# Performance work log

Hardware: AMD Instinct MI355X
Metric: run time of the kernel (lower is better)

## Reference

```python
import jax, jax.numpy as jnp
import numpy as np

B, T, C, H = 4, 2048, 1024, 16
HD = C // H

def setup_inputs() -> dict:
    key = jax.random.key(0)
    ks = jax.random.split(key, 9)
    s = 1.0 / np.sqrt(C)
    return {
        'x':  jax.random.normal(ks[0], (B, T, C), jnp.float32),
        'Wq': jax.random.normal(ks[1], (C, C), jnp.float32) * s,
        'bq': jnp.zeros((C,), jnp.float32),
        'Wk': jax.random.normal(ks[2], (C, C), jnp.float32) * s,
        'bk': jnp.zeros((C,), jnp.float32),
        'Wv': jax.random.normal(ks[3], (C, C), jnp.float32) * s,
        'bv': jnp.zeros((C,), jnp.float32),
        'Wo': jax.random.normal(ks[4], (C, C), jnp.float32) * s,
        'bo': jnp.zeros((C,), jnp.float32),
    }

def reference(x, Wq, bq, Wk, bk, Wv, bv, Wo, bo):
    Bx, Tx, Cx = x.shape
    # projections (torch Linear: x @ W.T + b); split heads -> (B,H,T,HD)
    def heads(y):
        return y.reshape(Bx, Tx, H, HD).transpose(0, 2, 1, 3)
    q = heads(x @ Wq.T + bq)
    k = heads(x @ Wk.T + bk)
    v = heads(x @ Wv.T + bv)
    # NOTE: original scales by 1/sqrt(embedding_dim), not head_dim
    scale = 1.0 / jnp.sqrt(jnp.asarray(Cx, x.dtype))
    att = jnp.einsum('bhqd,bhkd->bhqk', q, k) * scale
    mask = jnp.tril(jnp.ones((Tx, Tx), dtype=bool))
    att = jnp.where(mask, att, jnp.asarray(-jnp.inf, att.dtype))
    att = jax.nn.softmax(att, axis=-1)
    y = jnp.einsum('bhqk,bhkd->bhqd', att, v)
    y = y.transpose(0, 2, 1, 3).reshape(Bx, Tx, Cx)
    return y @ Wo.T + bo
```

## Files before the change

### kernel.cpp

```cpp
#include <hip/hip_runtime.h>
#include <hip/hip_bf16.h>
#include <stdint.h>

#define NB 4
#define NT 2048
#define NC 1024
#define NH 16
#define NHD 64
#define NM (NB*NT)

typedef __attribute__((ext_vector_type(8))) __bf16 bf16x8;
typedef __attribute__((ext_vector_type(4))) float floatx4;
typedef __attribute__((ext_vector_type(8))) unsigned short ushortx8;

#define AS1(p) ((const __attribute__((address_space(1))) void*)(p))
#define AS3(p) ((__attribute__((address_space(3))) void*)(p))

__device__ __forceinline__ unsigned short f2bf(float f) {
    union { float f; unsigned int u; } v; v.f = f;
    unsigned int u = v.u;
    return (unsigned short)((u + 0x7FFFu + ((u >> 16) & 1u)) >> 16);
}
__device__ __forceinline__ unsigned int pk2(float lo, float hi) {
    union { float f; unsigned int u; } a, b; a.f = hi; b.f = lo;
    return __builtin_amdgcn_perm(a.u, b.u, 0x07060302u);
}


__global__ void cast_all(const float* __restrict__ x,
                         const float* __restrict__ w0, const float* __restrict__ w1,
                         const float* __restrict__ w2, const float* __restrict__ w3,
                         unsigned short* __restrict__ xo,
                         unsigned short* __restrict__ o0, unsigned short* __restrict__ o1,
                         unsigned short* __restrict__ o2, unsigned short* __restrict__ o3)
{
    const int wid  = (blockIdx.x * blockDim.x + threadIdx.x) >> 6;
    const int lane = threadIdx.x & 63;
    const float* in; unsigned short* out; int tile;
    if (wid < 16384) { in = x; out = xo; tile = wid; }
    else {
        const int t = wid - 16384;
        tile = t & 2047;
        switch (t >> 11) {
            case 0: in = w0; out = o0; break;
            case 1: in = w1; out = o1; break;
            case 2: in = w2; out = o2; break;
            default: in = w3; out = o3; break;
        }
    }
    const int R = tile >> 5, C = tile & 31;
    const float* src = in + ((size_t)(R*16 + (lane >> 2)))*1024 + C*32 + (lane & 3)*8;
    const floatx4 v0 = *(const floatx4*)src;
    const floatx4 v1 = *(const floatx4*)(src + 4);
    ushortx8 o;
    o[0] = f2bf(v0[0]); o[1] = f2bf(v0[1]); o[2] = f2bf(v0[2]); o[3] = f2bf(v0[3]);
    o[4] = f2bf(v1[0]); o[5] = f2bf(v1[1]); o[6] = f2bf(v1[2]); o[7] = f2bf(v1[3]);
    *(ushortx8*)&out[(size_t)tile*512 + (((lane & 3)*16 + (lane >> 2)))*8] = o;
}

#define TM 128
#define BK 32

template<int MODE, int TN_>
__device__ __forceinline__ void gemm_core(
    const unsigned short* __restrict__ A,
    const unsigned short* __restrict__ W,
    const float* __restrict__ bias,
    void* __restrict__ Out,
    unsigned short* As, unsigned short* Bs,
    int m_base, int n_base, float oscale)
{
    constexpr int NI  = TN_ / 32;
    constexpr int TB4 = TN_ / 64;
    constexpr int BHALF = TN_ * 32;

    const int tid  = threadIdx.x;
    const int lane = tid & 63;
    const int wv   = tid >> 6;
    const int quad = lane >> 4;
    const int l16  = lane & 15;
    const int wm = (wv >> 1) * 64;
    const int wn = (wv & 1) * (TN_ / 2);

    floatx4 acc[4][NI];
    #pragma unroll
    for (int i = 0; i < 4; ++i)
        #pragma unroll
        for (int j = 0; j < NI; ++j)
            acc[i][j] = (floatx4){0.f, 0.f, 0.f, 0.f};

    const int kct = NC >> 5;

    const unsigned short* At = A + ((size_t)((m_base >> 4) + wv*2) * kct) * 512 + (size_t)lane*8;
    const unsigned short* Wt = W + ((size_t)((n_base >> 4) + wv*TB4) * kct) * 512 + (size_t)lane*8;
    const size_t rstride = (size_t)kct * 512;

    #pragma unroll
    for (int i = 0; i < 2; ++i)
        __builtin_amdgcn_global_load_lds(AS1(At + i*rstride),
                                         AS3(&As[(wv*2 + i)*512]), 16, 0, 0);
    #pragma unroll
    for (int i = 0; i < TB4; ++i)
        __builtin_amdgcn_global_load_lds(AS1(Wt + i*rstride),
                                         AS3(&Bs[(wv*TB4 + i)*512]), 16, 0, 0);

    #pragma unroll 1
    for (int kt = 0; kt < 32; ++kt) {
        const int curA = (kt & 1) ? 4096 : 0;
        const int nxtA = 4096 - curA;
        const int curB = (kt & 1) ? BHALF : 0;
        const int nxtB = BHALF - curB;
        if (kt < 31) {
            #pragma unroll
            for (int i = 0; i < 2; ++i)
                __builtin_amdgcn_global_load_lds(
                    AS1(At + (size_t)(kt+1)*512 + i*rstride),
                    AS3(&As[nxtA + (wv*2 + i)*512]), 16, 0, 0);
            #pragma unroll
            for (int i = 0; i < TB4; ++i)
                __builtin_amdgcn_global_load_lds(
                    AS1(Wt + (size_t)(kt+1)*512 + i*rstride),
                    AS3(&Bs[nxtB + (wv*TB4 + i)*512]), 16, 0, 0);
            if constexpr (TN_ == 128)
                asm volatile("s_waitcnt vmcnt(4)" ::: "memory");
            else
                asm volatile("s_waitcnt vmcnt(3)" ::: "memory");
        } else {
            asm volatile("s_waitcnt vmcnt(0)" ::: "memory");
        }
        __builtin_amdgcn_s_barrier();

        bf16x8 af[4], bfr[NI];
        #pragma unroll
        for (int mi = 0; mi < 4; ++mi)
            af[mi] = *(const bf16x8*)&As[curA + ((wv >> 1)*4 + mi)*512 + lane*8];
        #pragma unroll
        for (int ni = 0; ni < NI; ++ni)
            bfr[ni] = *(const bf16x8*)&Bs[curB + ((wv & 1)*NI + ni)*512 + lane*8];

        #pragma unroll
        for (int mi = 0; mi < 4; ++mi)
            #pragma unroll
            for (int ni = 0; ni < NI; ++ni) {
                if (MODE == 1)
                    acc[mi][ni] = __builtin_amdgcn_mfma_f32_16x16x32_bf16(
                        bfr[ni], af[mi], acc[mi][ni], 0, 0, 0);
                else
                    acc[mi][ni] = __builtin_amdgcn_mfma_f32_16x16x32_bf16(
                        af[mi], bfr[ni], acc[mi][ni], 0, 0, 0);
            }
        __builtin_amdgcn_s_barrier();
    }

    #pragma unroll
    for (int mi = 0; mi < 4; ++mi) {
        #pragma unroll
        for (int ni = 0; ni < NI; ++ni) {
            if (MODE == 0) {
                const int col = n_base + wn + ni*16 + l16;
                const float bv = bias[col & 1023];
                #pragma unroll
                for (int r = 0; r < 4; ++r) {
                    const int row = m_base + wm + mi*16 + quad*4 + r;
                    ((float*)Out)[(size_t)row * NC + col] =
                        (acc[mi][ni][r] + bv) * oscale;
                }
            } else if (MODE == 1) {
                const int d0 = n_base + wn + ni*16 + quad*4;
                const int t  = m_base + wm + mi*16 + l16;
                const float4 b4 = *(const float4*)&bias[d0];
                const int bb = t >> 11, tt = t & (NT - 1);
                const int h  = (d0 >> 6) & (NH - 1), dd0 = d0 & 63;
                const int bh = bb * NH + h;
                const size_t idx0 =
                    ((size_t)((bh*128 + (tt >> 4))*2 + (dd0 >> 5)))*512
                    + (size_t)((((dd0 >> 3) & 3)*16 + (tt & 15))*8 + (dd0 & 7));
                ushort4 st;
                st.x = f2bf((acc[mi][ni][0] + b4.x) * oscale);
                st.y = f2bf((acc[mi][ni][1] + b4.y) * oscale);
                st.z = f2bf((acc[mi][ni][2] + b4.z) * oscale);
                st.w = f2bf((acc[mi][ni][3] + b4.w) * oscale);
                *(ushort4*)&((unsigned short*)Out)[idx0] = st;
            } else {
                const int col = n_base + wn + ni*16 + l16;
                const float bv = bias[col & 1023];
                const int row0 = m_base + wm + mi*16 + quad*4;
                const int bb = row0 >> 11, t0 = row0 & (NT - 1);
                const int h  = (col >> 6) & (NH - 1), hd = col & 63;
                const int bh = bb * NH + h;
                const int tk0 = t0 & 31;
                const int qv  = (tk0 >> 2) & 3;
                const int jv0 = (tk0 >> 4) << 2;
                const size_t idx0 =
                    ((size_t)((bh*64 + (t0 >> 5))*4 + (hd >> 4)))*512
                    + (size_t)((qv*16 + (hd & 15))*8 + jv0);
                ushort4 st;
                st.x = f2bf((acc[mi][ni][0] + bv) * oscale);
                st.y = f2bf((acc[mi][ni][1] + bv) * oscale);
                st.z = f2bf((acc[mi][ni][2] + bv) * oscale);
                st.w = f2bf((acc[mi][ni][3] + bv) * oscale);
                *(ushort4*)&((unsigned short*)Out)[idx0] = st;
            }
        }
    }
}

#define QSCALE (0.03125f * 1.44269504088896340736f)

__global__ __launch_bounds__(256) void gemm_qkv(
    const unsigned short* __restrict__ A,
    const unsigned short* __restrict__ Wq, const unsigned short* __restrict__ Wk,
    const unsigned short* __restrict__ Wv,
    const float* __restrict__ bq, const float* __restrict__ bk,
    const float* __restrict__ bv,
    unsigned short* __restrict__ Qo, unsigned short* __restrict__ Ko,
    unsigned short* __restrict__ Vo)
{
    __shared__ __align__(16) unsigned short As[2*TM*BK];
    __shared__ __align__(16) unsigned short Bs[2*128*BK];
    const int wi = blockIdx.y >> 3;
    const int n_base = (blockIdx.y & 7) * 128;
    const int m_base = blockIdx.x * TM;
    if (wi == 0)
        gemm_core<1,128>(A, Wq, bq, Qo, As, Bs, m_base, n_base, QSCALE);
    else if (wi == 1)
        gemm_core<1,128>(A, Wk, bk, Ko, As, Bs, m_base, n_base, 1.0f);
    else
        gemm_core<2,128>(A, Wv, bv, Vo, As, Bs, m_base, n_base, 1.0f);
}

__global__ __launch_bounds__(256) void gemm_out(
    const unsigned short* __restrict__ A,
    const unsigned short* __restrict__ W,
    const float* __restrict__ bias,
    float* __restrict__ Out)
{
    __shared__ __align__(16) unsigned short As[2*TM*BK];
    __shared__ __align__(16) unsigned short Bs[2*64*BK];
    gemm_core<0,64>(A, W, bias, Out, As, Bs, blockIdx.x * TM, blockIdx.y * 64, 1.0f);
}

__device__ __forceinline__ void attn_tile(
    const bf16x8 kf[4][2], const bf16x8 vf[4][2],
    const bf16x8 q[4], floatx4 o[2][4], float l[2],
    bool diag, bool skiphi, int q0, int j0, int quad, int l16)
{
    #pragma unroll
    for (int sub = 0; sub < 2; ++sub) {
        const bf16x8 qx0 = q[sub*2];
        const bf16x8 qx1 = q[sub*2 + 1];

        floatx4 s[4];
        __builtin_amdgcn_s_setprio(1);
        #pragma unroll
        for (int ct = 0; ct < 2; ++ct) {
            s[ct] = (floatx4){0.f,0.f,0.f,0.f};
            s[ct] = __builtin_amdgcn_mfma_f32_16x16x32_bf16(kf[ct][0], qx0, s[ct], 0,0,0);
            s[ct] = __builtin_amdgcn_mfma_f32_16x16x32_bf16(kf[ct][1], qx1, s[ct], 0,0,0);
        }
        if (!skiphi) {
            #pragma unroll
            for (int ct = 2; ct < 4; ++ct) {
                s[ct] = (floatx4){0.f,0.f,0.f,0.f};
                s[ct] = __builtin_amdgcn_mfma_f32_16x16x32_bf16(kf[ct][0], qx0, s[ct], 0,0,0);
                s[ct] = __builtin_amdgcn_mfma_f32_16x16x32_bf16(kf[ct][1], qx1, s[ct], 0,0,0);
            }
        }
        __builtin_amdgcn_s_setprio(0);

        float p[4][4];
        float psum[4];
        const int row = q0 + sub*16 + l16;
        #pragma unroll
        for (int ct = 0; ct < 2; ++ct) {
            if (!diag) {
                #pragma unroll
                for (int r = 0; r < 4; ++r)
                    p[ct][r] = __builtin_amdgcn_exp2f(s[ct][r]);
            } else {
                #pragma unroll
                for (int r = 0; r < 4; ++r) {
                    const int key = j0 + ct*16 + quad*4 + r;
                    p[ct][r] = (key <= row) ? __builtin_amdgcn_exp2f(s[ct][r]) : 0.f;
                }
            }
            psum[ct] = (p[ct][0] + p[ct][1]) + (p[ct][2] + p[ct][3]);
        }
        if (!skiphi) {
            #pragma unroll
            for (int ct = 2; ct < 4; ++ct) {
                if (!diag) {
                    #pragma unroll
                    for (int r = 0; r < 4; ++r)
                        p[ct][r] = __builtin_amdgcn_exp2f(s[ct][r]);
                } else {
                    #pragma unroll
                    for (int r = 0; r < 4; ++r) {
                        const int key = j0 + ct*16 + quad*4 + r;
                        p[ct][r] = (key <= row) ? __builtin_amdgcn_exp2f(s[ct][r]) : 0.f;
                    }
                }
                psum[ct] = (p[ct][0] + p[ct][1]) + (p[ct][2] + p[ct][3]);
            }
            l[sub] += (psum[0] + psum[1]) + (psum[2] + psum[3]);
        } else {
            l[sub] += psum[0] + psum[1];
        }

        union { bf16x8 v; unsigned int u[4]; } pf0;
        pf0.u[0] = pk2(p[0][0], p[0][1]); pf0.u[1] = pk2(p[0][2], p[0][3]);
        pf0.u[2] = pk2(p[1][0], p[1][1]); pf0.u[3] = pk2(p[1][2], p[1][3]);

        __builtin_amdgcn_s_setprio(1);
        #pragma unroll
        for (int nt = 0; nt < 4; ++nt)
            o[sub][nt] = __builtin_amdgcn_mfma_f32_16x16x32_bf16(vf[nt][0], pf0.v, o[sub][nt], 0,0,0);
        __builtin_amdgcn_s_setprio(0);

        if (!skiphi) {
            union { bf16x8 v; unsigned int u[4]; } pf1;
            pf1.u[0] = pk2(p[2][0], p[2][1]); pf1.u[1] = pk2(p[2][2], p[2][3]);
            pf1.u[2] = pk2(p[3][0], p[3][1]); pf1.u[3] = pk2(p[3][2], p[3][3]);
            __builtin_amdgcn_s_setprio(1);
            #pragma unroll
            for (int nt = 0; nt < 4; ++nt)
                o[sub][nt] = __builtin_amdgcn_mfma_f32_16x16x32_bf16(vf[nt][1], pf1.v, o[sub][nt], 0,0,0);
            __builtin_amdgcn_s_setprio(0);
        }
    }
}

__device__ __forceinline__ void attn_store(
    unsigned short* __restrict__ Y, const floatx4 o[2][4], const float l[2],
    int q0, int b, int h, int quad, int l16)
{
    float la = l[0], lb = l[1];
    la += __shfl_xor(la, 16); la += __shfl_xor(la, 32);
    lb += __shfl_xor(lb, 16); lb += __shfl_xor(lb, 32);
    const float ia = 1.0f / la, ib = 1.0f / lb;
    const size_t Rbase = (size_t)((b*NT + q0) >> 4);
    const int cg = (quad >> 1), co = (quad & 1)*4;
    #pragma unroll
    for (int nt = 0; nt < 4; ++nt) {
        const size_t base = ((Rbase*32 + h*2 + (nt >> 1))*512)
                          + (size_t)((((nt & 1)*2 + cg)*16 + l16)*8 + co);
        ushort4 wa, wb;
        wa.x = f2bf(o[0][nt][0]*ia); wa.y = f2bf(o[0][nt][1]*ia);
        wa.z = f2bf(o[0][nt][2]*ia); wa.w = f2bf(o[0][nt][3]*ia);
        wb.x = f2bf(o[1][nt][0]*ib); wb.y = f2bf(o[1][nt][1]*ib);
        wb.z = f2bf(o[1][nt][2]*ib); wb.w = f2bf(o[1][nt][3]*ib);
        *(ushort4*)&Y[base]         = wa;
        *(ushort4*)&Y[base + 16384] = wb;
    }
}

__device__ __forceinline__ void attn_pair(
    const unsigned short* __restrict__ Qf,
    const unsigned short* __restrict__ Kf,
    const unsigned short* __restrict__ Vf,
    unsigned short* __restrict__ Y,
    int bh, int stA, int stB, int lane)
{
    const int quad = lane >> 4, l16 = lane & 15;
    const int b = bh >> 4, h = bh & (NH - 1);
    const int q0A = stA * 32, q0B = stB * 32;
    const int FA = q0A >> 6, FB = q0B >> 6;
    const bool skA = (q0A & 32) == 0;
    const bool skB = (q0B & 32) == 0;

    const size_t qbA = ((size_t)(bh*128 + stA*2))*1024 + (size_t)lane*8;
    const size_t qbB = ((size_t)(bh*128 + stB*2))*1024 + (size_t)lane*8;
    bf16x8 qA[4], qB[4];
    qA[0] = *(const bf16x8*)&Qf[qbA];
    qA[1] = *(const bf16x8*)&Qf[qbA + 512];
    qA[2] = *(const bf16x8*)&Qf[qbA + 1024];
    qA[3] = *(const bf16x8*)&Qf[qbA + 1536];
    qB[0] = *(const bf16x8*)&Qf[qbB];
    qB[1] = *(const bf16x8*)&Qf[qbB + 512];
    qB[2] = *(const bf16x8*)&Qf[qbB + 1024];
    qB[3] = *(const bf16x8*)&Qf[qbB + 1536];

    const unsigned short* kp = Kf + (size_t)bh*131072 + (size_t)lane*8;
    const unsigned short* vp = Vf + (size_t)bh*131072 + (size_t)lane*8;

    floatx4 oA[2][4], oB[2][4];
    float lA[2] = {0.f, 0.f}, lB[2] = {0.f, 0.f};
    #pragma unroll
    for (int s2 = 0; s2 < 2; ++s2)
        #pragma unroll
        for (int nt = 0; nt < 4; ++nt) {
            oA[s2][nt] = (floatx4){0.f,0.f,0.f,0.f};
            oB[s2][nt] = (floatx4){0.f,0.f,0.f,0.f};
        }

    for (int f = 0; f <= FB; ++f) {
        const int j0 = f * 64;
        bf16x8 kf[4][2], vf[4][2];
        const unsigned short* kt = kp + (size_t)f * 4096;
        #pragma unroll
        for (int ct = 0; ct < 4; ++ct) {
            kf[ct][0] = *(const bf16x8*)&kt[ct*1024];
            kf[ct][1] = *(const bf16x8*)&kt[ct*1024 + 512];
        }
        const unsigned short* vt = vp + (size_t)f * 4096;
        #pragma unroll
        for (int nt = 0; nt < 4; ++nt) {
            vf[nt][0] = *(const bf16x8*)&vt[nt*512];
            vf[nt][1] = *(const bf16x8*)&vt[2048 + nt*512];
        }

        if (f <= FA)
            attn_tile(kf, vf, qA, oA, lA, f == FA, (f == FA) && skA,
                      q0A, j0, quad, l16);
        attn_tile(kf, vf, qB, oB, lB, f == FB, (f == FB) && skB,
                  q0B, j0, quad, l16);
    }

    attn_store(Y, oA, lA, q0A, b, h, quad, l16);
    attn_store(Y, oB, lB, q0B, b, h, quad, l16);
}

__global__ __launch_bounds__(256, 2) void flash_attn(
    const unsigned short* __restrict__ Qf,
    const unsigned short* __restrict__ Kf,
    const unsigned short* __restrict__ Vf,
    unsigned short* __restrict__ Y)
{
    const int tid  = threadIdx.x;
    const int wave = tid >> 6;
    const int lane = tid & 63;
    const int L  = blockIdx.x;
    const int bh = (L & 7) * 8 + ((L >> 3) & 7);
    const int g  = L >> 6;
    const int x  = (g < 4) ? g : 11 - g;
    const int w  = x * 4 + wave;
    attn_pair(Qf, Kf, Vf, Y, bh, w, 63 - w, lane);
}

extern "C" void kernel_launch(void* const* d_in, const int* in_sizes, int n_in,
                              void* d_out, int out_size, void* d_ws, size_t ws_size,
                              hipStream_t stream) {
    const float* x  = (const float*)d_in[0];
    const float* Wq = (const float*)d_in[1];
    const float* bq = (const float*)d_in[2];
    const float* Wk = (const float*)d_in[3];
    const float* bk = (const float*)d_in[4];
    const float* Wv = (const float*)d_in[5];
    const float* bv = (const float*)d_in[6];
    const float* Wo = (const float*)d_in[7];
    const float* bo = (const float*)d_in[8];

    char* ws = (char*)d_ws;
    size_t off = 0;
    auto alloc = [&](size_t bytes) -> void* {
        void* p = ws + off;
        off += (bytes + 255) & ~(size_t)255;
        return p;
    };
    unsigned short* xb  = (unsigned short*)alloc((size_t)NM * NC * 2);
    unsigned short* Wqb = (unsigned short*)alloc((size_t)NC * NC * 2);
    unsigned short* Wkb = (unsigned short*)alloc((size_t)NC * NC * 2);
    unsigned short* Wvb = (unsigned short*)alloc((size_t)NC * NC * 2);
    unsigned short* Wob = (unsigned short*)alloc((size_t)NC * NC * 2);
    unsigned short* Qb  = (unsigned short*)alloc((size_t)NM * NC * 2);
    unsigned short* Kb  = (unsigned short*)alloc((size_t)NM * NC * 2);
    unsigned short* Vtb = (unsigned short*)alloc((size_t)NM * NC * 2);
    unsigned short* Yb  = (unsigned short*)alloc((size_t)NM * NC * 2);

    cast_all<<<(24576*64)/256, 256, 0, stream>>>(
        x, Wq, Wk, Wv, Wo, xb, Wqb, Wkb, Wvb, Wob);

    gemm_qkv<<<dim3(NM / TM, 24), 256, 0, stream>>>(
        xb, Wqb, Wkb, Wvb, bq, bk, bv, Qb, Kb, Vtb);

    flash_attn<<<dim3(512), 256, 0, stream>>>(Qb, Kb, Vtb, Yb);

    gemm_out<<<dim3(NM / TM, NC / 64), 256, 0, stream>>>(Yb, Wob, bo, (float*)d_out);
}
```

Measured before the change: 230.7 us.

## Replace paired causal q-tile scheduling with one tile per wave, heavy-first order

Each wave previously handled two complementary 32-row query tiles (w and 63-w) to balance causal work while sharing K/V loads. Now each wave processes a single query tile, the grid doubles to 1024 blocks, launch bounds allow 3 blocks per CU, and blocks are ordered so the longest causal tiles are scheduled first. This aims for more occupancy and fewer registers per wave, at the cost of losing K/V load sharing between the paired tiles and relying on the hardware scheduler for load balance.

```diff
diff --git a/kernel.cpp b/kernel.cpp
--- a/kernel.cpp
+++ b/kernel.cpp
@@ -354,46 +354,38 @@
     }
 }
 
-__device__ __forceinline__ void attn_pair(
+__device__ __forceinline__ void attn_one(
     const unsigned short* __restrict__ Qf,
     const unsigned short* __restrict__ Kf,
     const unsigned short* __restrict__ Vf,
     unsigned short* __restrict__ Y,
-    int bh, int stA, int stB, int lane)
+    int bh, int st, int lane)
 {
     const int quad = lane >> 4, l16 = lane & 15;
     const int b = bh >> 4, h = bh & (NH - 1);
-    const int q0A = stA * 32, q0B = stB * 32;
-    const int FA = q0A >> 6, FB = q0B >> 6;
-    const bool skA = (q0A & 32) == 0;
-    const bool skB = (q0B & 32) == 0;
-
-    const size_t qbA = ((size_t)(bh*128 + stA*2))*1024 + (size_t)lane*8;
-    const size_t qbB = ((size_t)(bh*128 + stB*2))*1024 + (size_t)lane*8;
-    bf16x8 qA[4], qB[4];
-    qA[0] = *(const bf16x8*)&Qf[qbA];
-    qA[1] = *(const bf16x8*)&Qf[qbA + 512];
-    qA[2] = *(const bf16x8*)&Qf[qbA + 1024];
-    qA[3] = *(const bf16x8*)&Qf[qbA + 1536];
-    qB[0] = *(const bf16x8*)&Qf[qbB];
-    qB[1] = *(const bf16x8*)&Qf[qbB + 512];
-    qB[2] = *(const bf16x8*)&Qf[qbB + 1024];
-    qB[3] = *(const bf16x8*)&Qf[qbB + 1536];
+    const int q0 = st * 32;
+    const int F = q0 >> 6;
+    const bool sk = (q0 & 32) == 0;
+
+    const size_t qb = ((size_t)(bh*128 + st*2))*1024 + (size_t)lane*8;
+    bf16x8 q[4];
+    q[0] = *(const bf16x8*)&Qf[qb];
+    q[1] = *(const bf16x8*)&Qf[qb + 512];
+    q[2] = *(const bf16x8*)&Qf[qb + 1024];
+    q[3] = *(const bf16x8*)&Qf[qb + 1536];
 
     const unsigned short* kp = Kf + (size_t)bh*131072 + (size_t)lane*8;
     const unsigned short* vp = Vf + (size_t)bh*131072 + (size_t)lane*8;
 
-    floatx4 oA[2][4], oB[2][4];
-    float lA[2] = {0.f, 0.f}, lB[2] = {0.f, 0.f};
+    floatx4 o[2][4];
+    float l[2] = {0.f, 0.f};
     #pragma unroll
     for (int s2 = 0; s2 < 2; ++s2)
         #pragma unroll
-        for (int nt = 0; nt < 4; ++nt) {
-            oA[s2][nt] = (floatx4){0.f,0.f,0.f,0.f};
-            oB[s2][nt] = (floatx4){0.f,0.f,0.f,0.f};
-        }
-
-    for (int f = 0; f <= FB; ++f) {
+        for (int nt = 0; nt < 4; ++nt)
+            o[s2][nt] = (floatx4){0.f,0.f,0.f,0.f};
+
+    for (int f = 0; f <= F; ++f) {
         const int j0 = f * 64;
         bf16x8 kf[4][2], vf[4][2];
         const unsigned short* kt = kp + (size_t)f * 4096;
@@ -408,19 +400,13 @@
             vf[nt][0] = *(const bf16x8*)&vt[nt*512];
             vf[nt][1] = *(const bf16x8*)&vt[2048 + nt*512];
         }
-
-        if (f <= FA)
-            attn_tile(kf, vf, qA, oA, lA, f == FA, (f == FA) && skA,
-                      q0A, j0, quad, l16);
-        attn_tile(kf, vf, qB, oB, lB, f == FB, (f == FB) && skB,
-                  q0B, j0, quad, l16);
-    }
-
-    attn_store(Y, oA, lA, q0A, b, h, quad, l16);
-    attn_store(Y, oB, lB, q0B, b, h, quad, l16);
-}
-
-__global__ __launch_bounds__(256, 2) void flash_attn(
+        attn_tile(kf, vf, q, o, l, f == F, (f == F) && sk, q0, j0, quad, l16);
+    }
+
+    attn_store(Y, o, l, q0, b, h, quad, l16);
+}
+
+__global__ __launch_bounds__(256, 3) void flash_attn(
     const unsigned short* __restrict__ Qf,
     const unsigned short* __restrict__ Kf,
     const unsigned short* __restrict__ Vf,
@@ -432,9 +418,8 @@
     const int L  = blockIdx.x;
     const int bh = (L & 7) * 8 + ((L >> 3) & 7);
     const int g  = L >> 6;
-    const int x  = (g < 4) ? g : 11 - g;
-    const int w  = x * 4 + wave;
-    attn_pair(Qf, Kf, Vf, Y, bh, w, 63 - w, lane);
+    const int st = (15 - g) * 4 + wave;
+    attn_one(Qf, Kf, Vf, Y, bh, st, lane);
 }
 
 extern "C" void kernel_launch(void* const* d_in, const int* in_sizes, int n_in,
@@ -473,7 +458,7 @@
     gemm_qkv<<<dim3(NM / TM, 24), 256, 0, stream>>>(
         xb, Wqb, Wkb, Wvb, bq, bk, bv, Qb, Kb, Vtb);
 
-    flash_attn<<<dim3(512), 256, 0, stream>>>(Qb, Kb, Vtb, Yb);
+    flash_attn<<<dim3(1024), 256, 0, stream>>>(Qb, Kb, Vtb, Yb);
 
     gemm_out<<<dim3(NM / TM, NC / 64), 256, 0, stream>>>(Yb, Wob, bo, (float*)d_out);
 }
```

Measured after the change: 239.7 us. 1.04x slower.
